# Optimization experiments

Hardware: AMD Instinct MI355X
Metric: run time of the kernel (lower is better)

## Reference

```python
import jax, jax.numpy as jnp
import numpy as np

SOBEL_X = jnp.array([[-1., 0., 1.], [-2., 0., 2.], [-1., 0., 1.]], dtype=jnp.float32).reshape(1, 1, 3, 3)
SOBEL_Y = jnp.array([[-1., -2., -1.], [0., 0., 0.], [1., 2., 1.]], dtype=jnp.float32).reshape(1, 1, 3, 3)


def _gray(x):
    # x: (B, 3, H, W) -> (B, 1, H, W)
    if x.shape[1] == 3:
        return 0.299 * x[:, 0:1] + 0.587 * x[:, 1:2] + 0.114 * x[:, 2:3]
    return x


def _edges(g):
    # g: (B, 1, H, W); 3x3 Sobel convs with padding 1 (cross-correlation, like torch conv2d)
    dn = ('NCHW', 'OIHW', 'NCHW')
    ex = jax.lax.conv_general_dilated(g, SOBEL_X, (1, 1), ((1, 1), (1, 1)), dimension_numbers=dn)
    ey = jax.lax.conv_general_dilated(g, SOBEL_Y, (1, 1), ((1, 1), (1, 1)), dimension_numbers=dn)
    return jnp.sqrt(ex * ex + ey * ey)


def setup_inputs() -> dict:
    key = jax.random.key(0)
    k1, k2 = jax.random.split(key)
    pred = jax.random.normal(k1, (32, 3, 512, 512), dtype=jnp.float32)
    target = jax.random.normal(k2, (32, 3, 512, 512), dtype=jnp.float32)
    return {"pred": pred, "target": target}


def reference(pred, target):
    pred_edges = _edges(_gray(pred))
    target_edges = _edges(_gray(target))
    return jnp.mean(jnp.abs(pred_edges - target_edges))
```

## Files before the change

kernel.cpp:

```cpp
#include <hip/hip_runtime.h>


#define BATCH 32
#define HH 512
#define WW 512
#define SROWS 8
#define IMG ((size_t)HH * WW)

__global__ void zero_out_kernel(float* out) { out[0] = 0.0f; }

#define TOGRAY(d4, dl, dr, r4, g4, b4, rl, gl, bl, rr, gr, br) do {   \
    d4.x = 0.299f * r4.x + 0.587f * g4.x + 0.114f * b4.x;             \
    d4.y = 0.299f * r4.y + 0.587f * g4.y + 0.114f * b4.y;             \
    d4.z = 0.299f * r4.z + 0.587f * g4.z + 0.114f * b4.z;             \
    d4.w = 0.299f * r4.w + 0.587f * g4.w + 0.114f * b4.w;             \
    dl   = 0.299f * (rl) + 0.587f * (gl) + 0.114f * (bl);             \
    dr   = 0.299f * (rr) + 0.587f * (gr) + 0.114f * (br);             \
} while (0)

#define MAG(a0, a1, a2, b0, b2, c0, c1, c2)                            \
    ({ float ex_ = ((a2) - (a0)) + 2.0f * ((b2) - (b0)) + ((c2) - (c0)); \
       float ey_ = ((c0) - (a0)) + 2.0f * ((c1) - (a1)) + ((c2) - (a2)); \
       sqrtf(ex_ * ex_ + ey_ * ey_); })

__global__ __launch_bounds__(256) void edge_loss_kernel(
    const float* __restrict__ pred,
    const float* __restrict__ target,
    float* __restrict__ out)
{
    const int tid  = threadIdx.x;
    const int lane = tid & 63;
    const int wav  = tid >> 6;
    const int colhalf = blockIdx.x;
    const int band = blockIdx.y * 4 + wav;
    const int b    = blockIdx.z;

    const int y0 = band * SROWS;
    const int c0 = colhalf * 256 + lane * 4;

    const float* pb = pred   + (size_t)b * 3 * IMG;
    const float* tb = target + (size_t)b * 3 * IMG;

    const bool okl = (c0 >= 1);
    const bool okr = (c0 <= WW - 5);
    const int  xlo = okl ? -1 : 0;
    const int  xro = okr ?  4 : 3;

    float4 cpr, cpg, cpb, ctr, ctg, ctb;
    float  cprl, cpgl, cpbl, cprr, cpgr, cpbr;
    float  ctrl_, ctgl, ctbl, ctrr, ctgr, ctbr;

#define LOADROW(gy_) do {                                              \
    const int gy = (gy_);                                              \
    if ((unsigned)gy < (unsigned)HH) {                                 \
        const float* rp = pb + (size_t)gy * WW + c0;                   \
        const float* rt = tb + (size_t)gy * WW + c0;                   \
        cpr = *(const float4*)(rp);                                    \
        cpg = *(const float4*)(rp + IMG);                              \
        cpb = *(const float4*)(rp + 2 * IMG);                          \
        ctr = *(const float4*)(rt);                                    \
        ctg = *(const float4*)(rt + IMG);                              \
        ctb = *(const float4*)(rt + 2 * IMG);                          \
        float al0 = rp[xlo], al1 = rp[IMG + xlo], al2 = rp[2 * IMG + xlo]; \
        float ar0 = rp[xro], ar1 = rp[IMG + xro], ar2 = rp[2 * IMG + xro]; \
        float bl0 = rt[xlo], bl1 = rt[IMG + xlo], bl2 = rt[2 * IMG + xlo]; \
        float br0 = rt[xro], br1 = rt[IMG + xro], br2 = rt[2 * IMG + xro]; \
        cprl = okl ? al0 : 0.f; cpgl = okl ? al1 : 0.f; cpbl = okl ? al2 : 0.f; \
        cprr = okr ? ar0 : 0.f; cpgr = okr ? ar1 : 0.f; cpbr = okr ? ar2 : 0.f; \
        ctrl_ = okl ? bl0 : 0.f; ctgl = okl ? bl1 : 0.f; ctbl = okl ? bl2 : 0.f; \
        ctrr = okr ? br0 : 0.f; ctgr = okr ? br1 : 0.f; ctbr = okr ? br2 : 0.f; \
    } else {                                                           \
        cpr = cpg = cpb = make_float4(0.f, 0.f, 0.f, 0.f);             \
        ctr = ctg = ctb = make_float4(0.f, 0.f, 0.f, 0.f);             \
        cprl = cpgl = cpbl = cprr = cpgr = cpbr = 0.f;                 \
        ctrl_ = ctgl = ctbl = ctrr = ctgr = ctbr = 0.f;                \
    }                                                                  \
} while (0)

#define GRAY_P(d4, dl, dr) TOGRAY(d4, dl, dr, cpr, cpg, cpb, cprl, cpgl, cpbl, cprr, cpgr, cpbr)
#define GRAY_T(d4, dl, dr) TOGRAY(d4, dl, dr, ctr, ctg, ctb, ctrl_, ctgl, ctbl, ctrr, ctgr, ctbr)

    float4 pA4, pB4, pC4, tA4, tB4, tC4;
    float  pAl, pAr, pBl, pBr, pCl, pCr;
    float  tAl, tAr, tBl, tBr, tCl, tCr;

    LOADROW(y0 - 1);
    GRAY_P(pA4, pAl, pAr);
    GRAY_T(tA4, tAl, tAr);
    LOADROW(y0);
    GRAY_P(pB4, pBl, pBr);
    GRAY_T(tB4, tBl, tBr);
    LOADROW(y0 + 1);

    float lsum = 0.0f;

    #pragma unroll
    for (int i = 0; i < SROWS; ++i) {
        GRAY_P(pC4, pCl, pCr);
        GRAY_T(tC4, tCl, tCr);

        if (i < SROWS - 1) LOADROW(y0 + 2 + i);
        __builtin_amdgcn_sched_barrier(0);

        float ep, et;
        ep = MAG(pAl,   pA4.x, pA4.y,  pBl,   pB4.y,  pCl,   pC4.x, pC4.y);
        et = MAG(tAl,   tA4.x, tA4.y,  tBl,   tB4.y,  tCl,   tC4.x, tC4.y);
        lsum += fabsf(ep - et);
        ep = MAG(pA4.x, pA4.y, pA4.z,  pB4.x, pB4.z,  pC4.x, pC4.y, pC4.z);
        et = MAG(tA4.x, tA4.y, tA4.z,  tB4.x, tB4.z,  tC4.x, tC4.y, tC4.z);
        lsum += fabsf(ep - et);
        ep = MAG(pA4.y, pA4.z, pA4.w,  pB4.y, pB4.w,  pC4.y, pC4.z, pC4.w);
        et = MAG(tA4.y, tA4.z, tA4.w,  tB4.y, tB4.w,  tC4.y, tC4.z, tC4.w);
        lsum += fabsf(ep - et);
        ep = MAG(pA4.z, pA4.w, pAr,    pB4.z, pBr,    pC4.z, pC4.w, pCr);
        et = MAG(tA4.z, tA4.w, tAr,    tB4.z, tBr,    tC4.z, tC4.w, tCr);
        lsum += fabsf(ep - et);

        pA4 = pB4; pAl = pBl; pAr = pBr;
        pB4 = pC4; pBl = pCl; pBr = pCr;
        tA4 = tB4; tAl = tBl; tAr = tBr;
        tB4 = tC4; tBl = tCl; tBr = tCr;
    }

    #pragma unroll
    for (int off = 32; off > 0; off >>= 1)
        lsum += __shfl_down(lsum, off, 64);

    if (lane == 0) {
        const float inv_n = 1.0f / ((float)BATCH * HH * WW);
        atomicAdd(out, lsum * inv_n);
    }
}

extern "C" void kernel_launch(void* const* d_in, const int* in_sizes, int n_in,
                              void* d_out, int out_size, void* d_ws, size_t ws_size,
                              hipStream_t stream) {
    const float* pred   = (const float*)d_in[0];
    const float* target = (const float*)d_in[1];
    float* out = (float*)d_out;

    zero_out_kernel<<<1, 1, 0, stream>>>(out);

    dim3 grid(2, 16, BATCH);
    edge_loss_kernel<<<grid, 256, 0, stream>>>(pred, target, out);
}
```

Before: 241.6 us.

## Widen each lane to 8 columns, get halos via shuffles, double-buffer row loads

Each wavefront now covers a full 512-wide row, with every lane handling 8 columns loaded as two float4s. The left and right halo pixels come from cross-lane shuffles of the computed grayscale values instead of extra scalar global loads. Row loads are double-buffered across two register sets so the next row's fetch is issued before the current row's grayscale and Sobel math. The goal is fewer memory instructions and more loads in flight per thread, at the cost of higher register pressure and half as many blocks in the grid.

```diff
diff --git a/kernel.cpp b/kernel.cpp
--- a/kernel.cpp
+++ b/kernel.cpp
@@ -4,24 +4,107 @@
 #define BATCH 32
 #define HH 512
 #define WW 512
-#define SROWS 8
+#define S 8
 #define IMG ((size_t)HH * WW)
 
 __global__ void zero_out_kernel(float* out) { out[0] = 0.0f; }
 
-#define TOGRAY(d4, dl, dr, r4, g4, b4, rl, gl, bl, rr, gr, br) do {   \
-    d4.x = 0.299f * r4.x + 0.587f * g4.x + 0.114f * b4.x;             \
-    d4.y = 0.299f * r4.y + 0.587f * g4.y + 0.114f * b4.y;             \
-    d4.z = 0.299f * r4.z + 0.587f * g4.z + 0.114f * b4.z;             \
-    d4.w = 0.299f * r4.w + 0.587f * g4.w + 0.114f * b4.w;             \
-    dl   = 0.299f * (rl) + 0.587f * (gl) + 0.114f * (bl);             \
-    dr   = 0.299f * (rr) + 0.587f * (gr) + 0.114f * (br);             \
-} while (0)
-
-#define MAG(a0, a1, a2, b0, b2, c0, c1, c2)                            \
+#define MAG(a0, a1, a2, b0, b2, c0, c1, c2)                              \
     ({ float ex_ = ((a2) - (a0)) + 2.0f * ((b2) - (b0)) + ((c2) - (c0)); \
        float ey_ = ((c0) - (a0)) + 2.0f * ((c1) - (a1)) + ((c2) - (a2)); \
        sqrtf(ex_ * ex_ + ey_ * ey_); })
+
+#define LOADSET(P, gy_) do {                                           \
+    const int gy__ = (gy_);                                            \
+    if ((unsigned)gy__ < (unsigned)HH) {                               \
+        const float* rp__ = pbase + (size_t)gy__ * WW + cx;            \
+        const float* rt__ = tbase + (size_t)gy__ * WW + cx;            \
+        P##pr0 = *(const float4*)(rp__);                               \
+        P##pr1 = *(const float4*)(rp__ + 4);                           \
+        P##pg0 = *(const float4*)(rp__ + IMG);                         \
+        P##pg1 = *(const float4*)(rp__ + IMG + 4);                     \
+        P##pb0 = *(const float4*)(rp__ + 2 * IMG);                     \
+        P##pb1 = *(const float4*)(rp__ + 2 * IMG + 4);                 \
+        P##tr0 = *(const float4*)(rt__);                               \
+        P##tr1 = *(const float4*)(rt__ + 4);                           \
+        P##tg0 = *(const float4*)(rt__ + IMG);                         \
+        P##tg1 = *(const float4*)(rt__ + IMG + 4);                     \
+        P##tb0 = *(const float4*)(rt__ + 2 * IMG);                     \
+        P##tb1 = *(const float4*)(rt__ + 2 * IMG + 4);                 \
+    } else {                                                           \
+        const float4 z__ = make_float4(0.f, 0.f, 0.f, 0.f);            \
+        P##pr0 = z__; P##pr1 = z__; P##pg0 = z__; P##pg1 = z__;        \
+        P##pb0 = z__; P##pb1 = z__; P##tr0 = z__; P##tr1 = z__;        \
+        P##tg0 = z__; P##tg1 = z__; P##tb0 = z__; P##tb1 = z__;        \
+    }                                                                  \
+    __builtin_amdgcn_sched_barrier(0);                                 \
+} while (0)
+
+#define GRAYSET(R, P) do {                                                  \
+    R##p0 = 0.299f * P##pr0.x + 0.587f * P##pg0.x + 0.114f * P##pb0.x;      \
+    R##p1 = 0.299f * P##pr0.y + 0.587f * P##pg0.y + 0.114f * P##pb0.y;      \
+    R##p2 = 0.299f * P##pr0.z + 0.587f * P##pg0.z + 0.114f * P##pb0.z;      \
+    R##p3 = 0.299f * P##pr0.w + 0.587f * P##pg0.w + 0.114f * P##pb0.w;      \
+    R##p4 = 0.299f * P##pr1.x + 0.587f * P##pg1.x + 0.114f * P##pb1.x;      \
+    R##p5 = 0.299f * P##pr1.y + 0.587f * P##pg1.y + 0.114f * P##pb1.y;      \
+    R##p6 = 0.299f * P##pr1.z + 0.587f * P##pg1.z + 0.114f * P##pb1.z;      \
+    R##p7 = 0.299f * P##pr1.w + 0.587f * P##pg1.w + 0.114f * P##pb1.w;      \
+    R##t0 = 0.299f * P##tr0.x + 0.587f * P##tg0.x + 0.114f * P##tb0.x;      \
+    R##t1 = 0.299f * P##tr0.y + 0.587f * P##tg0.y + 0.114f * P##tb0.y;      \
+    R##t2 = 0.299f * P##tr0.z + 0.587f * P##tg0.z + 0.114f * P##tb0.z;      \
+    R##t3 = 0.299f * P##tr0.w + 0.587f * P##tg0.w + 0.114f * P##tb0.w;      \
+    R##t4 = 0.299f * P##tr1.x + 0.587f * P##tg1.x + 0.114f * P##tb1.x;      \
+    R##t5 = 0.299f * P##tr1.y + 0.587f * P##tg1.y + 0.114f * P##tb1.y;      \
+    R##t6 = 0.299f * P##tr1.z + 0.587f * P##tg1.z + 0.114f * P##tb1.z;      \
+    R##t7 = 0.299f * P##tr1.w + 0.587f * P##tg1.w + 0.114f * P##tb1.w;      \
+    { float sl_ = __shfl_up(R##p7, 1, 64);                                  \
+      float sr_ = __shfl_down(R##p0, 1, 64);                                \
+      R##pl = (lane == 0)  ? 0.f : sl_;                                     \
+      R##pr = (lane == 63) ? 0.f : sr_;                                     \
+      float tl_ = __shfl_up(R##t7, 1, 64);                                  \
+      float tr_ = __shfl_down(R##t0, 1, 64);                                \
+      R##tl = (lane == 0)  ? 0.f : tl_;                                     \
+      R##tr = (lane == 63) ? 0.f : tr_; }                                   \
+} while (0)
+
+#define SOBELROW() do {                                              \
+    float ep_, et_;                                                  \
+    ep_ = MAG(Apl, Ap0, Ap1,  Bpl, Bp1,  Cpl, Cp0, Cp1);             \
+    et_ = MAG(Atl, At0, At1,  Btl, Bt1,  Ctl, Ct0, Ct1);             \
+    lsum += fabsf(ep_ - et_);                                        \
+    ep_ = MAG(Ap0, Ap1, Ap2,  Bp0, Bp2,  Cp0, Cp1, Cp2);             \
+    et_ = MAG(At0, At1, At2,  Bt0, Bt2,  Ct0, Ct1, Ct2);             \
+    lsum += fabsf(ep_ - et_);                                        \
+    ep_ = MAG(Ap1, Ap2, Ap3,  Bp1, Bp3,  Cp1, Cp2, Cp3);             \
+    et_ = MAG(At1, At2, At3,  Bt1, Bt3,  Ct1, Ct2, Ct3);             \
+    lsum += fabsf(ep_ - et_);                                        \
+    ep_ = MAG(Ap2, Ap3, Ap4,  Bp2, Bp4,  Cp2, Cp3, Cp4);             \
+    et_ = MAG(At2, At3, At4,  Bt2, Bt4,  Ct2, Ct3, Ct4);             \
+    lsum += fabsf(ep_ - et_);                                        \
+    ep_ = MAG(Ap3, Ap4, Ap5,  Bp3, Bp5,  Cp3, Cp4, Cp5);             \
+    et_ = MAG(At3, At4, At5,  Bt3, Bt5,  Ct3, Ct4, Ct5);             \
+    lsum += fabsf(ep_ - et_);                                        \
+    ep_ = MAG(Ap4, Ap5, Ap6,  Bp4, Bp6,  Cp4, Cp5, Cp6);             \
+    et_ = MAG(At4, At5, At6,  Bt4, Bt6,  Ct4, Ct5, Ct6);             \
+    lsum += fabsf(ep_ - et_);                                        \
+    ep_ = MAG(Ap5, Ap6, Ap7,  Bp5, Bp7,  Cp5, Cp6, Cp7);             \
+    et_ = MAG(At5, At6, At7,  Bt5, Bt7,  Ct5, Ct6, Ct7);             \
+    lsum += fabsf(ep_ - et_);                                        \
+    ep_ = MAG(Ap6, Ap7, Apr,  Bp6, Bpr,  Cp6, Cp7, Cpr);             \
+    et_ = MAG(At6, At7, Atr,  Bt6, Btr,  Ct6, Ct7, Ctr);             \
+    lsum += fabsf(ep_ - et_);                                        \
+} while (0)
+
+#define ROTATE() do {                                                \
+    Ap0=Bp0; Ap1=Bp1; Ap2=Bp2; Ap3=Bp3; Ap4=Bp4; Ap5=Bp5; Ap6=Bp6; Ap7=Bp7; \
+    Apl=Bpl; Apr=Bpr;                                                \
+    At0=Bt0; At1=Bt1; At2=Bt2; At3=Bt3; At4=Bt4; At5=Bt5; At6=Bt6; At7=Bt7; \
+    Atl=Btl; Atr=Btr;                                                \
+    Bp0=Cp0; Bp1=Cp1; Bp2=Cp2; Bp3=Cp3; Bp4=Cp4; Bp5=Cp5; Bp6=Cp6; Bp7=Cp7; \
+    Bpl=Cpl; Bpr=Cpr;                                                \
+    Bt0=Ct0; Bt1=Ct1; Bt2=Ct2; Bt3=Ct3; Bt4=Ct4; Bt5=Ct5; Bt6=Ct6; Bt7=Ct7; \
+    Btl=Ctl; Btr=Ctr;                                                \
+} while (0)
 
 __global__ __launch_bounds__(256) void edge_loss_kernel(
     const float* __restrict__ pred,
@@ -31,95 +114,45 @@
     const int tid  = threadIdx.x;
     const int lane = tid & 63;
     const int wav  = tid >> 6;
-    const int colhalf = blockIdx.x;
-    const int band = blockIdx.y * 4 + wav;
-    const int b    = blockIdx.z;
+    const int band = blockIdx.x * 4 + wav;
+    const int b    = blockIdx.y;
+    const int y0   = band * S;
+    const int cx   = lane * 8;
 
-    const int y0 = band * SROWS;
-    const int c0 = colhalf * 256 + lane * 4;
+    const float* pbase = pred   + (size_t)b * 3 * IMG;
+    const float* tbase = target + (size_t)b * 3 * IMG;
 
-    const float* pb = pred   + (size_t)b * 3 * IMG;
-    const float* tb = target + (size_t)b * 3 * IMG;
+    float4 Xpr0, Xpr1, Xpg0, Xpg1, Xpb0, Xpb1;
+    float4 Xtr0, Xtr1, Xtg0, Xtg1, Xtb0, Xtb1;
+    float4 Ypr0, Ypr1, Ypg0, Ypg1, Ypb0, Ypb1;
+    float4 Ytr0, Ytr1, Ytg0, Ytg1, Ytb0, Ytb1;
 
-    const bool okl = (c0 >= 1);
-    const bool okr = (c0 <= WW - 5);
-    const int  xlo = okl ? -1 : 0;
-    const int  xro = okr ?  4 : 3;
+    float Ap0,Ap1,Ap2,Ap3,Ap4,Ap5,Ap6,Ap7, Apl,Apr;
+    float At0,At1,At2,At3,At4,At5,At6,At7, Atl,Atr;
+    float Bp0,Bp1,Bp2,Bp3,Bp4,Bp5,Bp6,Bp7, Bpl,Bpr;
+    float Bt0,Bt1,Bt2,Bt3,Bt4,Bt5,Bt6,Bt7, Btl,Btr;
+    float Cp0,Cp1,Cp2,Cp3,Cp4,Cp5,Cp6,Cp7, Cpl,Cpr;
+    float Ct0,Ct1,Ct2,Ct3,Ct4,Ct5,Ct6,Ct7, Ctl,Ctr;
 
-    float4 cpr, cpg, cpb, ctr, ctg, ctb;
-    float  cprl, cpgl, cpbl, cprr, cpgr, cpbr;
-    float  ctrl_, ctgl, ctbl, ctrr, ctgr, ctbr;
-
-#define LOADROW(gy_) do {                                              \
-    const int gy = (gy_);                                              \
-    if ((unsigned)gy < (unsigned)HH) {                                 \
-        const float* rp = pb + (size_t)gy * WW + c0;                   \
-        const float* rt = tb + (size_t)gy * WW + c0;                   \
-        cpr = *(const float4*)(rp);                                    \
-        cpg = *(const float4*)(rp + IMG);                              \
-        cpb = *(const float4*)(rp + 2 * IMG);                          \
-        ctr = *(const float4*)(rt);                                    \
-        ctg = *(const float4*)(rt + IMG);                              \
-        ctb = *(const float4*)(rt + 2 * IMG);                          \
-        float al0 = rp[xlo], al1 = rp[IMG + xlo], al2 = rp[2 * IMG + xlo]; \
-        float ar0 = rp[xro], ar1 = rp[IMG + xro], ar2 = rp[2 * IMG + xro]; \
-        float bl0 = rt[xlo], bl1 = rt[IMG + xlo], bl2 = rt[2 * IMG + xlo]; \
-        float br0 = rt[xro], br1 = rt[IMG + xro], br2 = rt[2 * IMG + xro]; \
-        cprl = okl ? al0 : 0.f; cpgl = okl ? al1 : 0.f; cpbl = okl ? al2 : 0.f; \
-        cprr = okr ? ar0 : 0.f; cpgr = okr ? ar1 : 0.f; cpbr = okr ? ar2 : 0.f; \
-        ctrl_ = okl ? bl0 : 0.f; ctgl = okl ? bl1 : 0.f; ctbl = okl ? bl2 : 0.f; \
-        ctrr = okr ? br0 : 0.f; ctgr = okr ? br1 : 0.f; ctbr = okr ? br2 : 0.f; \
-    } else {                                                           \
-        cpr = cpg = cpb = make_float4(0.f, 0.f, 0.f, 0.f);             \
-        ctr = ctg = ctb = make_float4(0.f, 0.f, 0.f, 0.f);             \
-        cprl = cpgl = cpbl = cprr = cpgr = cpbr = 0.f;                 \
-        ctrl_ = ctgl = ctbl = ctrr = ctgr = ctbr = 0.f;                \
-    }                                                                  \
-} while (0)
-
-#define GRAY_P(d4, dl, dr) TOGRAY(d4, dl, dr, cpr, cpg, cpb, cprl, cpgl, cpbl, cprr, cpgr, cpbr)
-#define GRAY_T(d4, dl, dr) TOGRAY(d4, dl, dr, ctr, ctg, ctb, ctrl_, ctgl, ctbl, ctrr, ctgr, ctbr)
-
-    float4 pA4, pB4, pC4, tA4, tB4, tC4;
-    float  pAl, pAr, pBl, pBr, pCl, pCr;
-    float  tAl, tAr, tBl, tBr, tCl, tCr;
-
-    LOADROW(y0 - 1);
-    GRAY_P(pA4, pAl, pAr);
-    GRAY_T(tA4, tAl, tAr);
-    LOADROW(y0);
-    GRAY_P(pB4, pBl, pBr);
-    GRAY_T(tB4, tBl, tBr);
-    LOADROW(y0 + 1);
+    LOADSET(X, y0 - 1);
+    LOADSET(Y, y0);
+    GRAYSET(A, X);
+    LOADSET(X, y0 + 1);
+    GRAYSET(B, Y);
 
     float lsum = 0.0f;
 
     #pragma unroll
-    for (int i = 0; i < SROWS; ++i) {
-        GRAY_P(pC4, pCl, pCr);
-        GRAY_T(tC4, tCl, tCr);
-
-        if (i < SROWS - 1) LOADROW(y0 + 2 + i);
-        __builtin_amdgcn_sched_barrier(0);
-
-        float ep, et;
-        ep = MAG(pAl,   pA4.x, pA4.y,  pBl,   pB4.y,  pCl,   pC4.x, pC4.y);
-        et = MAG(tAl,   tA4.x, tA4.y,  tBl,   tB4.y,  tCl,   tC4.x, tC4.y);
-        lsum += fabsf(ep - et);
-        ep = MAG(pA4.x, pA4.y, pA4.z,  pB4.x, pB4.z,  pC4.x, pC4.y, pC4.z);
-        et = MAG(tA4.x, tA4.y, tA4.z,  tB4.x, tB4.z,  tC4.x, tC4.y, tC4.z);
-        lsum += fabsf(ep - et);
-        ep = MAG(pA4.y, pA4.z, pA4.w,  pB4.y, pB4.w,  pC4.y, pC4.z, pC4.w);
-        et = MAG(tA4.y, tA4.z, tA4.w,  tB4.y, tB4.w,  tC4.y, tC4.z, tC4.w);
-        lsum += fabsf(ep - et);
-        ep = MAG(pA4.z, pA4.w, pAr,    pB4.z, pBr,    pC4.z, pC4.w, pCr);
-        et = MAG(tA4.z, tA4.w, tAr,    tB4.z, tBr,    tC4.z, tC4.w, tCr);
-        lsum += fabsf(ep - et);
-
-        pA4 = pB4; pAl = pBl; pAr = pBr;
-        pB4 = pC4; pBl = pCl; pBr = pCr;
-        tA4 = tB4; tAl = tBl; tAr = tBr;
-        tB4 = tC4; tBl = tCl; tBr = tCr;
+    for (int i = 0; i < S; ++i) {
+        if (i & 1) {
+            if (i < S - 1) LOADSET(X, y0 + 2 + i);
+            GRAYSET(C, Y);
+        } else {
+            if (i < S - 1) LOADSET(Y, y0 + 2 + i);
+            GRAYSET(C, X);
+        }
+        SOBELROW();
+        ROTATE();
     }
 
     #pragma unroll
@@ -141,6 +174,6 @@
 
     zero_out_kernel<<<1, 1, 0, stream>>>(out);
 
-    dim3 grid(2, 16, BATCH);
+    dim3 grid(16, BATCH, 1);
     edge_loss_kernel<<<grid, 256, 0, stream>>>(pred, target, out);
 }
```

Result: no change. 241.1 us (-0.2%).
